# Kernel tuning notes

Measured on AMD Instinct MI355X. Metric: run time of the kernel, lower is better.

## Reference

```python
import jax, jax.numpy as jnp
import numpy as np
from jax import lax

N_LINKS = 10000
N_PATHS = 100000
PATH_LEN = 8   # max_seq_len (all paths padded to this)
H = 32         # link/path state dim and GRU hidden size
RD = 8         # readout dim
T = 8          # message-passing rounds


def setup_inputs() -> dict:
    key = jax.random.key(0)
    ks = jax.random.split(key, 20)
    E = N_PATHS * PATH_LEN
    links = jax.random.randint(ks[0], (E,), 0, N_LINKS)
    paths = jnp.repeat(jnp.arange(N_PATHS), PATH_LEN)
    seqs = jnp.tile(jnp.arange(PATH_LEN), N_PATHS)
    link_capacity = jax.random.uniform(ks[1], (N_LINKS,), dtype=jnp.float32)
    bandwith = jax.random.uniform(ks[2], (N_PATHS,), dtype=jnp.float32)
    s = 1.0 / np.sqrt(H)
    u = lambda k, shp: jax.random.uniform(k, shp, minval=-s, maxval=s, dtype=jnp.float32)
    return {
        'links': links, 'paths': paths, 'seqs': seqs,
        'link_capacity': link_capacity, 'bandwith': bandwith,
        # path GRU (p_U) params, torch layout: [3H, in] with gate order r,z,n
        'p_Wih': u(ks[3], (3 * H, H)), 'p_Whh': u(ks[4], (3 * H, H)),
        'p_bih': u(ks[5], (3 * H,)), 'p_bhh': u(ks[6], (3 * H,)),
        # link GRU (l_U) params
        'l_Wih': u(ks[7], (3 * H, H)), 'l_Whh': u(ks[8], (3 * H, H)),
        'l_bih': u(ks[9], (3 * H,)), 'l_bhh': u(ks[10], (3 * H,)),
        # readout MLP
        'W1': u(ks[11], (RD, H)), 'b1': u(ks[12], (RD,)),
        'W2': u(ks[13], (RD, RD)), 'b2': u(ks[14], (RD,)),
        'W3': u(ks[15], (1, RD)), 'b3': u(ks[16], (1,)),
    }


def gru_cell(x, h, Wih, Whh, bih, bhh):
    # torch GRU cell: gates in order (reset, update, new)
    gi = x @ Wih.T + bih   # [N, 3H]
    gh = h @ Whh.T + bhh   # [N, 3H]
    i_r, i_z, i_n = jnp.split(gi, 3, axis=-1)
    h_r, h_z, h_n = jnp.split(gh, 3, axis=-1)
    r = jax.nn.sigmoid(i_r + h_r)
    z = jax.nn.sigmoid(i_z + h_z)
    n = jnp.tanh(i_n + r * h_n)
    return (1.0 - z) * n + z * h


def reference(links, paths, seqs, link_capacity, bandwith,
              p_Wih, p_Whh, p_bih, p_bhh,
              l_Wih, l_Whh, l_bih, l_bhh,
              W1, b1, W2, b2, W3, b3):
    dt = link_capacity.dtype
    # initial states: feature 0 is capacity / bandwidth, rest zeros
    link_state = jnp.concatenate(
        [link_capacity[:, None], jnp.zeros((N_LINKS, H - 1), dt)], axis=1)
    path_state = jnp.concatenate(
        [bandwith[:, None], jnp.zeros((N_PATHS, H - 1), dt)], axis=1)

    def path_step(h, x_t):
        h2 = gru_cell(x_t, h, p_Wih, p_Whh, p_bih, p_bhh)
        return h2, h2

    for _ in range(T):
        # gather link states onto path hops: [E, H]
        gathered = link_state[links]
        # scatter into dense padded path-RNN input [n_paths, L, H]
        rnn_in = jnp.zeros((N_PATHS, PATH_LEN, H), dt).at[paths, seqs].set(gathered)
        # path GRU over the padded sequence, initial hidden = path_state
        path_state, hs = lax.scan(path_step, path_state,
                                  jnp.swapaxes(rnn_in, 0, 1))  # hs: [L, n_paths, H]
        # per-hop messages back to links, then scatter-add per link
        link_msgs = hs[seqs, paths]                            # [E, H]
        agg = jax.ops.segment_sum(link_msgs, links, num_segments=N_LINKS)
        # link GRU single step: input = aggregated message, hidden = link_state
        link_state = gru_cell(agg, link_state, l_Wih, l_Whh, l_bih, l_bhh)

    # readout MLP on final path state
    x = jax.nn.relu(path_state @ W1.T + b1)
    x = jax.nn.relu(x @ W2.T + b2)
    return x @ W3.T + b3  # [n_paths, 1]
```

## Files before the change

### kernel.cpp

```cpp
#include <hip/hip_runtime.h>
#include <hip/hip_bf16.h>

#define NL 10000
#define NP 100000
#define PLEN 8
#define H 32
#define NROUNDS 8
#define E_TOT (NP * PLEN)

typedef float f2 __attribute__((ext_vector_type(2)));
typedef float f4 __attribute__((ext_vector_type(4)));
typedef short bh8 __attribute__((ext_vector_type(8)));

#define LINK_OFF   0
#define PATH_OFF   320000
#define AGG_OFF    3520000
#define WTS_OFF    3840000
#define PW_OFF     3853400
#define FLAG_OFF   3869000
#define INT_OFF    3870000
#define HS_OFF     4700032
#define WS_NEED_FLOATS (HS_OFF + (size_t)E_TOT * H)

#define LOG2E 1.44269504f

__device__ __forceinline__ float bf2f(unsigned short u) {
  union { unsigned int i; float f; } v; v.i = ((unsigned int)u) << 16; return v.f;
}
__device__ __forceinline__ float fast_exp2(float x) {
#if __has_builtin(__builtin_amdgcn_exp2f)
  return __builtin_amdgcn_exp2f(x);
#else
  return __expf(x * 0.69314718f);
#endif
}
__device__ __forceinline__ float fast_rcp(float x) {
#if __has_builtin(__builtin_amdgcn_rcpf)
  return __builtin_amdgcn_rcpf(x);
#else
  return 1.f / x;
#endif
}
__device__ __forceinline__ float fast_sigm(float x) {
  return fast_rcp(1.f + fast_exp2(-LOG2E * x));
}
__device__ __forceinline__ float fast_tanh2(float x) {
  return 1.f - 2.f * fast_rcp(1.f + fast_exp2((2.f * LOG2E) * x));
}
__device__ __forceinline__ float loadf(const void* p, long i, bool bf) {
  return bf ? bf2f(((const unsigned short*)p)[i]) : ((const float*)p)[i];
}

__device__ __forceinline__ void split8(f4 a, f4 b, bh8& hi, bh8& lo) {
  #pragma unroll
  for (int i = 0; i < 4; ++i) {
    unsigned ua = __float_as_uint(a[i]);
    float hfa = __uint_as_float(ua & 0xffff0000u);
    hi[i] = (short)(ua >> 16);
    lo[i] = (short)(__float_as_uint(a[i] - hfa) >> 16);
    unsigned ub = __float_as_uint(b[i]);
    float hfb = __uint_as_float(ub & 0xffff0000u);
    hi[4 + i] = (short)(ub >> 16);
    lo[4 + i] = (short)(__float_as_uint(b[i] - hfb) >> 16);
  }
}

__global__ void probe_dtype(const unsigned int* __restrict__ cap_words,
                            int* __restrict__ flag) {
  int lane = threadIdx.x;
  int c = 0;
  #pragma unroll
  for (int i = 0; i < 4; ++i) {
    unsigned int b = (cap_words[lane * 4 + i] >> 8) & 0xFF;
    if (b >= 0x30 && b < 0x40) ++c;
  }
  #pragma unroll
  for (int d = 32; d > 0; d >>= 1) c += __shfl_down(c, d);
  if (lane == 0) *flag = (c > 128) ? 1 : 0;
}

__device__ __forceinline__ void gru_cell_f2(const float* __restrict__ W,
                                            const f2 x[16], f2 h[16]) {
  const f2* Wih = (const f2*)W;
  const f2* Whh = (const f2*)(W + 3072);
  const float* bih = W + 6144;
  const float* bhh = W + 6240;
  f2 hn[16];
  #pragma unroll
  for (int jj = 0; jj < 16; ++jj) {
    #pragma unroll
    for (int s = 0; s < 2; ++s) {
      const int j = 2 * jj + s;
      f2 ar = {0.f, 0.f}, az = {0.f, 0.f}, an = {0.f, 0.f}, ah = {0.f, 0.f};
      #pragma unroll
      for (int k = 0; k < 16; ++k) {
        ar = __builtin_elementwise_fma(Wih[j * 16 + k], x[k], ar);
        ar = __builtin_elementwise_fma(Whh[j * 16 + k], h[k], ar);
        az = __builtin_elementwise_fma(Wih[(H + j) * 16 + k], x[k], az);
        az = __builtin_elementwise_fma(Whh[(H + j) * 16 + k], h[k], az);
        an = __builtin_elementwise_fma(Wih[(2 * H + j) * 16 + k], x[k], an);
        ah = __builtin_elementwise_fma(Whh[(2 * H + j) * 16 + k], h[k], ah);
      }
      float r = fast_sigm(ar.x + ar.y + bih[j] + bhh[j]);
      float z = fast_sigm(az.x + az.y + bih[H + j] + bhh[H + j]);
      float n = fast_tanh2(an.x + an.y + bih[2 * H + j] +
                           r * (ah.x + ah.y + bhh[2 * H + j]));
      float hold = (s == 0) ? h[jj].x : h[jj].y;
      float hv = n + z * (hold - n);
      if (s == 0) hn[jj].x = hv; else hn[jj].y = hv;
    }
  }
  #pragma unroll
  for (int k = 0; k < 16; ++k) h[k] = hn[k];
}

struct BfSeg { const void* src; int dstoff; int len; };
struct BfSegs { BfSeg s[14]; };
struct WPack { unsigned short* p[8]; };

__global__ void convert_weights(BfSegs segs, WPack wp, const int* __restrict__ flag,
                                float* __restrict__ dst) {
  const bool bf = (*flag != 0);
  const int si = blockIdx.x;
  const void* p = segs.s[si].src;
  const int off = segs.s[si].dstoff, len = segs.s[si].len;
  int hix = -1;
  if (si == 0) hix = 0; else if (si == 1) hix = 2;
  else if (si == 4) hix = 4; else if (si == 5) hix = 6;
  for (int i = threadIdx.x; i < len; i += blockDim.x) {
    float f = loadf(p, i, bf);
    dst[off + i] = f;
    if (hix >= 0) {
      unsigned u = __float_as_uint(f);
      float fh = __uint_as_float(u & 0xffff0000u);
      wp.p[hix][i] = (unsigned short)(u >> 16);
      wp.p[hix + 1][i] = (unsigned short)(__float_as_uint(f - fh) >> 16);
    }
  }
}

__global__ void init_states(const void* __restrict__ cap,
                            const void* __restrict__ bw,
                            const int* __restrict__ flag,
                            float* __restrict__ link_state,
                            unsigned short* __restrict__ lhi,
                            unsigned short* __restrict__ llo,
                            float* __restrict__ path_state) {
  const bool bf = (*flag != 0);
  int i = blockIdx.x * blockDim.x + threadIdx.x;
  if (i < NP * H) path_state[i] = ((i & (H - 1)) == 0) ? loadf(bw, i >> 5, bf) : 0.f;
  if (i < NL * H) {
    float v = ((i & (H - 1)) == 0) ? loadf(cap, i >> 5, bf) : 0.f;
    link_state[i] = v;
    unsigned u = __float_as_uint(v);
    float fh = __uint_as_float(u & 0xffff0000u);
    lhi[i] = (unsigned short)(u >> 16);
    llo[i] = (unsigned short)(__float_as_uint(v - fh) >> 16);
  }
}

__global__ void csr_count(const int* __restrict__ links, int* __restrict__ counts) {
  int e = blockIdx.x * blockDim.x + threadIdx.x;
  if (e < E_TOT) atomicAdd(&counts[links[e]], 1);
}

__global__ __launch_bounds__(256) void csr_scan(const int* __restrict__ counts,
                                                int* __restrict__ offsets,
                                                int* __restrict__ cursor) {
  __shared__ int part[256];
  const int t = threadIdx.x;
  const int base = t * 40;
  int s = 0;
  for (int i = 0; i < 40; ++i) {
    int idx = base + i;
    if (idx < NL) s += counts[idx];
  }
  part[t] = s;
  __syncthreads();
  for (int d = 1; d < 256; d <<= 1) {
    int v = (t >= d) ? part[t - d] : 0;
    __syncthreads();
    part[t] += v;
    __syncthreads();
  }
  int run = (t > 0) ? part[t - 1] : 0;
  for (int i = 0; i < 40; ++i) {
    int idx = base + i;
    if (idx < NL) {
      offsets[idx] = run;
      cursor[idx] = run;
      run += counts[idx];
    }
  }
  if (t == 255) offsets[NL] = run;
}

__global__ void csr_fill(const int* __restrict__ links, int* __restrict__ cursor,
                         int* __restrict__ edges) {
  int e = blockIdx.x * blockDim.x + threadIdx.x;
  if (e < E_TOT) {
    int l = links[e];
    int pos = atomicAdd(&cursor[l], 1);
    edges[pos] = e;
  }
}

__global__ __launch_bounds__(256) void path_round_mfma(
    const int* __restrict__ links,
    const unsigned short* __restrict__ lhi, const unsigned short* __restrict__ llo,
    float* __restrict__ path_state, float* __restrict__ hs,
    const float* __restrict__ W,
    const unsigned short* __restrict__ wih_hi, const unsigned short* __restrict__ wih_lo,
    const unsigned short* __restrict__ whh_hi, const unsigned short* __restrict__ whh_lo,
    int store_msgs) {
  __shared__ float lds_all[4 * 16 * 36];
  const int wv = threadIdx.x >> 6;
  const int tile = blockIdx.x * 4 + wv;
  if (tile >= NP / 16) return;
  const int p0 = tile * 16;
  const int lane = threadIdx.x & 63;
  const int c = lane & 15, q = lane >> 4, m = c;
  float* lds = lds_all + wv * (16 * 36);

  bh8 wihH[6], wihL[6], whhH[6], whhL[6];
  #pragma unroll
  for (int tn = 0; tn < 6; ++tn) {
    size_t o = (size_t)(tn * 16 + c) * H + q * 8;
    wihH[tn] = *(const bh8*)(wih_hi + o);
    wihL[tn] = *(const bh8*)(wih_lo + o);
    whhH[tn] = *(const bh8*)(whh_hi + o);
    whhL[tn] = *(const bh8*)(whh_lo + o);
  }
  const float* bih = W + 6144;
  const float* bhh = W + 6240;
  f4 bR[2], bZ[2], bI[2], bHn[2];
  #pragma unroll
  for (int u2 = 0; u2 < 2; ++u2) {
    int u = u2 * 16 + c;
    float vr = bih[u] + bhh[u];
    float vz = bih[32 + u] + bhh[32 + u];
    float vi = bih[64 + u];
    float vh = bhh[64 + u];
    bR[u2] = (f4){vr, vr, vr, vr};
    bZ[u2] = (f4){vz, vz, vz, vz};
    bI[u2] = (f4){vi, vi, vi, vi};
    bHn[u2] = (f4){vh, vh, vh, vh};
  }
  float hC[2][4];
  #pragma unroll
  for (int u2 = 0; u2 < 2; ++u2)
    #pragma unroll
    for (int rg = 0; rg < 4; ++rg)
      hC[u2][rg] = path_state[(size_t)(p0 + q * 4 + rg) * H + u2 * 16 + c];
  f4 hfa = *(const f4*)(path_state + (size_t)(p0 + m) * H + q * 8);
  f4 hfb = *(const f4*)(path_state + (size_t)(p0 + m) * H + q * 8 + 4);
  bh8 hhi, hlo;
  split8(hfa, hfb, hhi, hlo);
  int lk[PLEN];
  {
    const int4* lp = (const int4*)(links + (size_t)(p0 + m) * PLEN);
    int4 a = lp[0], b = lp[1];
    lk[0] = a.x; lk[1] = a.y; lk[2] = a.z; lk[3] = a.w;
    lk[4] = b.x; lk[5] = b.y; lk[6] = b.z; lk[7] = b.w;
  }
  bh8 xhi = *(const bh8*)(lhi + (size_t)lk[0] * H + q * 8);
  bh8 xlo = *(const bh8*)(llo + (size_t)lk[0] * H + q * 8);

  #pragma unroll 1
  for (int t = 0; t < PLEN; ++t) {
    bh8 xnhi, xnlo;
    if (t + 1 < PLEN) {
      xnhi = *(const bh8*)(lhi + (size_t)lk[t + 1] * H + q * 8);
      xnlo = *(const bh8*)(llo + (size_t)lk[t + 1] * H + q * 8);
    }
    f4 aR[2], aZ[2], aI[2], aHn[2];
    #pragma unroll
    for (int u2 = 0; u2 < 2; ++u2) {
      f4 a = bR[u2];
      a = __builtin_amdgcn_mfma_f32_16x16x32_bf16(xhi, wihH[u2], a, 0, 0, 0);
      a = __builtin_amdgcn_mfma_f32_16x16x32_bf16(hhi, whhH[u2], a, 0, 0, 0);
      a = __builtin_amdgcn_mfma_f32_16x16x32_bf16(xlo, wihH[u2], a, 0, 0, 0);
      a = __builtin_amdgcn_mfma_f32_16x16x32_bf16(hlo, whhH[u2], a, 0, 0, 0);
      a = __builtin_amdgcn_mfma_f32_16x16x32_bf16(xhi, wihL[u2], a, 0, 0, 0);
      a = __builtin_amdgcn_mfma_f32_16x16x32_bf16(hhi, whhL[u2], a, 0, 0, 0);
      aR[u2] = a;
      f4 b = bZ[u2];
      b = __builtin_amdgcn_mfma_f32_16x16x32_bf16(xhi, wihH[2 + u2], b, 0, 0, 0);
      b = __builtin_amdgcn_mfma_f32_16x16x32_bf16(hhi, whhH[2 + u2], b, 0, 0, 0);
      b = __builtin_amdgcn_mfma_f32_16x16x32_bf16(xlo, wihH[2 + u2], b, 0, 0, 0);
      b = __builtin_amdgcn_mfma_f32_16x16x32_bf16(hlo, whhH[2 + u2], b, 0, 0, 0);
      b = __builtin_amdgcn_mfma_f32_16x16x32_bf16(xhi, wihL[2 + u2], b, 0, 0, 0);
      b = __builtin_amdgcn_mfma_f32_16x16x32_bf16(hhi, whhL[2 + u2], b, 0, 0, 0);
      aZ[u2] = b;
      f4 ci = bI[u2];
      ci = __builtin_amdgcn_mfma_f32_16x16x32_bf16(xhi, wihH[4 + u2], ci, 0, 0, 0);
      ci = __builtin_amdgcn_mfma_f32_16x16x32_bf16(xlo, wihH[4 + u2], ci, 0, 0, 0);
      ci = __builtin_amdgcn_mfma_f32_16x16x32_bf16(xhi, wihL[4 + u2], ci, 0, 0, 0);
      aI[u2] = ci;
      f4 ch = bHn[u2];
      ch = __builtin_amdgcn_mfma_f32_16x16x32_bf16(hhi, whhH[4 + u2], ch, 0, 0, 0);
      ch = __builtin_amdgcn_mfma_f32_16x16x32_bf16(hlo, whhH[4 + u2], ch, 0, 0, 0);
      ch = __builtin_amdgcn_mfma_f32_16x16x32_bf16(hhi, whhL[4 + u2], ch, 0, 0, 0);
      aHn[u2] = ch;
    }
    #pragma unroll
    for (int u2 = 0; u2 < 2; ++u2)
      #pragma unroll
      for (int rg = 0; rg < 4; ++rg) {
        float rr = fast_sigm(aR[u2][rg]);
        float zz = fast_sigm(aZ[u2][rg]);
        float nn = fast_tanh2(fmaf(rr, aHn[u2][rg], aI[u2][rg]));
        float hv = fmaf(zz, hC[u2][rg] - nn, nn);
        hC[u2][rg] = hv;
        lds[(q * 4 + rg) * 36 + u2 * 16 + c] = hv;
      }
    __builtin_amdgcn_wave_barrier();
    __builtin_amdgcn_s_waitcnt(0xC07F);
    f4 ha = *(const f4*)(lds + m * 36 + q * 8);
    f4 hb = *(const f4*)(lds + m * 36 + q * 8 + 4);
    __builtin_amdgcn_wave_barrier();
    if (store_msgs) {
      float* hp = hs + ((size_t)(p0 + m) * PLEN + t) * H + q * 8;
      *(f4*)hp = ha;
      *(f4*)(hp + 4) = hb;
    }
    if (t + 1 < PLEN) {
      split8(ha, hb, hhi, hlo);
      xhi = xnhi; xlo = xnlo;
    } else {
      float* pp = path_state + (size_t)(p0 + m) * H + q * 8;
      *(f4*)pp = ha;
      *(f4*)(pp + 4) = hb;
    }
  }
}

__global__ __launch_bounds__(256) void agg_link_round(
    const int* __restrict__ offsets, const int* __restrict__ edges,
    const float* __restrict__ hs, float* __restrict__ link_state,
    unsigned short* __restrict__ lhi, unsigned short* __restrict__ llo,
    const float* __restrict__ W,
    const unsigned short* __restrict__ wih_hi, const unsigned short* __restrict__ wih_lo,
    const unsigned short* __restrict__ whh_hi, const unsigned short* __restrict__ whh_lo) {
  __shared__ float aggL[16 * 36];
  const int l0 = blockIdx.x * 16;
  const int elem = threadIdx.x & 31;
  #pragma unroll
  for (int li2 = 0; li2 < 2; ++li2) {
    const int li = (threadIdx.x >> 5) + li2 * 8;
    const int l = l0 + li;
    const int beg = offsets[l], end = offsets[l + 1];
    float s0 = 0.f, s1 = 0.f, s2 = 0.f, s3 = 0.f;
    int i = beg;
    for (; i + 3 < end; i += 4) {
      int e0 = edges[i], e1 = edges[i + 1], e2 = edges[i + 2], e3 = edges[i + 3];
      s0 += hs[(size_t)e0 * H + elem];
      s1 += hs[(size_t)e1 * H + elem];
      s2 += hs[(size_t)e2 * H + elem];
      s3 += hs[(size_t)e3 * H + elem];
    }
    for (; i < end; ++i) s0 += hs[(size_t)edges[i] * H + elem];
    aggL[li * 36 + elem] = (s0 + s1) + (s2 + s3);
  }
  __syncthreads();
  if (threadIdx.x >= 64) return;
  const int lane = threadIdx.x;
  const int c = lane & 15, q = lane >> 4, m = c;
  bh8 wihH[6], wihL[6], whhH[6], whhL[6];
  #pragma unroll
  for (int tn = 0; tn < 6; ++tn) {
    size_t o = (size_t)(tn * 16 + c) * H + q * 8;
    wihH[tn] = *(const bh8*)(wih_hi + o);
    wihL[tn] = *(const bh8*)(wih_lo + o);
    whhH[tn] = *(const bh8*)(whh_hi + o);
    whhL[tn] = *(const bh8*)(whh_lo + o);
  }
  const float* bih = W + 6144;
  const float* bhh = W + 6240;
  f4 bR[2], bZ[2], bI[2], bHn[2];
  #pragma unroll
  for (int u2 = 0; u2 < 2; ++u2) {
    int u = u2 * 16 + c;
    float vr = bih[u] + bhh[u];
    float vz = bih[32 + u] + bhh[32 + u];
    float vi = bih[64 + u];
    float vh = bhh[64 + u];
    bR[u2] = (f4){vr, vr, vr, vr};
    bZ[u2] = (f4){vz, vz, vz, vz};
    bI[u2] = (f4){vi, vi, vi, vi};
    bHn[u2] = (f4){vh, vh, vh, vh};
  }
  float hC[2][4];
  #pragma unroll
  for (int u2 = 0; u2 < 2; ++u2)
    #pragma unroll
    for (int rg = 0; rg < 4; ++rg)
      hC[u2][rg] = link_state[(size_t)(l0 + q * 4 + rg) * H + u2 * 16 + c];
  f4 xa = *(const f4*)(aggL + m * 36 + q * 8);
  f4 xb = *(const f4*)(aggL + m * 36 + q * 8 + 4);
  f4 hfa = *(const f4*)(link_state + (size_t)(l0 + m) * H + q * 8);
  f4 hfb = *(const f4*)(link_state + (size_t)(l0 + m) * H + q * 8 + 4);
  bh8 xhi, xlo, hhi, hlo;
  split8(xa, xb, xhi, xlo);
  split8(hfa, hfb, hhi, hlo);
  f4 aR[2], aZ[2], aI[2], aHn[2];
  #pragma unroll
  for (int u2 = 0; u2 < 2; ++u2) {
    f4 a = bR[u2];
    a = __builtin_amdgcn_mfma_f32_16x16x32_bf16(xhi, wihH[u2], a, 0, 0, 0);
    a = __builtin_amdgcn_mfma_f32_16x16x32_bf16(hhi, whhH[u2], a, 0, 0, 0);
    a = __builtin_amdgcn_mfma_f32_16x16x32_bf16(xlo, wihH[u2], a, 0, 0, 0);
    a = __builtin_amdgcn_mfma_f32_16x16x32_bf16(hlo, whhH[u2], a, 0, 0, 0);
    a = __builtin_amdgcn_mfma_f32_16x16x32_bf16(xhi, wihL[u2], a, 0, 0, 0);
    a = __builtin_amdgcn_mfma_f32_16x16x32_bf16(hhi, whhL[u2], a, 0, 0, 0);
    aR[u2] = a;
    f4 b = bZ[u2];
    b = __builtin_amdgcn_mfma_f32_16x16x32_bf16(xhi, wihH[2 + u2], b, 0, 0, 0);
    b = __builtin_amdgcn_mfma_f32_16x16x32_bf16(hhi, whhH[2 + u2], b, 0, 0, 0);
    b = __builtin_amdgcn_mfma_f32_16x16x32_bf16(xlo, wihH[2 + u2], b, 0, 0, 0);
    b = __builtin_amdgcn_mfma_f32_16x16x32_bf16(hlo, whhH[2 + u2], b, 0, 0, 0);
    b = __builtin_amdgcn_mfma_f32_16x16x32_bf16(xhi, wihL[2 + u2], b, 0, 0, 0);
    b = __builtin_amdgcn_mfma_f32_16x16x32_bf16(hhi, whhL[2 + u2], b, 0, 0, 0);
    aZ[u2] = b;
    f4 ci = bI[u2];
    ci = __builtin_amdgcn_mfma_f32_16x16x32_bf16(xhi, wihH[4 + u2], ci, 0, 0, 0);
    ci = __builtin_amdgcn_mfma_f32_16x16x32_bf16(xlo, wihH[4 + u2], ci, 0, 0, 0);
    ci = __builtin_amdgcn_mfma_f32_16x16x32_bf16(xhi, wihL[4 + u2], ci, 0, 0, 0);
    aI[u2] = ci;
    f4 ch = bHn[u2];
    ch = __builtin_amdgcn_mfma_f32_16x16x32_bf16(hhi, whhH[4 + u2], ch, 0, 0, 0);
    ch = __builtin_amdgcn_mfma_f32_16x16x32_bf16(hlo, whhH[4 + u2], ch, 0, 0, 0);
    ch = __builtin_amdgcn_mfma_f32_16x16x32_bf16(hhi, whhL[4 + u2], ch, 0, 0, 0);
    aHn[u2] = ch;
  }
  #pragma unroll
  for (int u2 = 0; u2 < 2; ++u2)
    #pragma unroll
    for (int rg = 0; rg < 4; ++rg) {
      float rr = fast_sigm(aR[u2][rg]);
      float zz = fast_sigm(aZ[u2][rg]);
      float nn = fast_tanh2(fmaf(rr, aHn[u2][rg], aI[u2][rg]));
      float hv = fmaf(zz, hC[u2][rg] - nn, nn);
      size_t idx = (size_t)(l0 + q * 4 + rg) * H + u2 * 16 + c;
      link_state[idx] = hv;
      unsigned u = __float_as_uint(hv);
      float fh = __uint_as_float(u & 0xffff0000u);
      lhi[idx] = (unsigned short)(u >> 16);
      llo[idx] = (unsigned short)(__float_as_uint(hv - fh) >> 16);
    }
}

__global__ __launch_bounds__(64) void path_round_atomic(
    const int* __restrict__ links, const float* __restrict__ link_state,
    float* __restrict__ path_state, float* __restrict__ agg,
    const float* __restrict__ W, int do_scatter) {
  int p = blockIdx.x * 64 + threadIdx.x;
  if (p >= NP) return;
  f2 h[16];
  const f2* ps2 = (const f2*)(path_state + (size_t)p * H);
  #pragma unroll
  for (int k = 0; k < 16; ++k) h[k] = ps2[k];
  int lk[PLEN];
  const int4* lp = (const int4*)(links + (size_t)p * PLEN);
  int4 la = lp[0], lb = lp[1];
  lk[0] = la.x; lk[1] = la.y; lk[2] = la.z; lk[3] = la.w;
  lk[4] = lb.x; lk[5] = lb.y; lk[6] = lb.z; lk[7] = lb.w;
  #pragma unroll 1
  for (int t = 0; t < PLEN; ++t) {
    const f2* xs = (const f2*)(link_state + (size_t)lk[t] * H);
    f2 x[16];
    #pragma unroll
    for (int k = 0; k < 16; ++k) x[k] = xs[k];
    gru_cell_f2(W, x, h);
    if (do_scatter) {
      float* dst = agg + (size_t)lk[t] * H;
      #pragma unroll
      for (int k = 0; k < 16; ++k) {
        unsafeAtomicAdd(dst + 2 * k, h[k].x);
        unsafeAtomicAdd(dst + 2 * k + 1, h[k].y);
      }
    }
  }
  f2* po = (f2*)(path_state + (size_t)p * H);
  #pragma unroll
  for (int k = 0; k < 16; ++k) po[k] = h[k];
}

__global__ __launch_bounds__(64) void link_round_scalar(
    const float* __restrict__ agg, float* __restrict__ link_state,
    const float* __restrict__ W) {
  int li = blockIdx.x * 64 + threadIdx.x;
  if (li >= NL) return;
  f2 x[16], h[16];
  const f2* xa = (const f2*)(agg + (size_t)li * H);
  f2* hsrow = (f2*)(link_state + (size_t)li * H);
  #pragma unroll
  for (int k = 0; k < 16; ++k) { x[k] = xa[k]; h[k] = hsrow[k]; }
  gru_cell_f2(W, x, h);
  #pragma unroll
  for (int k = 0; k < 16; ++k) hsrow[k] = h[k];
}

__global__ __launch_bounds__(256) void readout_kernel(
    const float* __restrict__ path_state, const float* __restrict__ W,
    const int* __restrict__ flag, void* __restrict__ out) {
  int p = blockIdx.x * 256 + threadIdx.x;
  if (p >= NP) return;
  const float* W1 = W;
  const float* b1 = W + 256;
  const float* W2 = W + 264;
  const float* b2 = W + 328;
  const float* W3 = W + 336;
  const float* b3 = W + 344;
  float xv[32];
  const float4* xp = (const float4*)(path_state + (size_t)p * H);
  #pragma unroll
  for (int k = 0; k < 8; ++k) {
    float4 v = xp[k];
    xv[4 * k] = v.x; xv[4 * k + 1] = v.y; xv[4 * k + 2] = v.z; xv[4 * k + 3] = v.w;
  }
  float y1[8];
  #pragma unroll
  for (int i = 0; i < 8; ++i) {
    float a = b1[i];
    #pragma unroll
    for (int k = 0; k < 32; ++k) a = fmaf(W1[i * 32 + k], xv[k], a);
    y1[i] = fmaxf(a, 0.f);
  }
  float y2[8];
  #pragma unroll
  for (int i = 0; i < 8; ++i) {
    float a = b2[i];
    #pragma unroll
    for (int k = 0; k < 8; ++k) a = fmaf(W2[i * 8 + k], y1[k], a);
    y2[i] = fmaxf(a, 0.f);
  }
  float o = b3[0];
  #pragma unroll
  for (int k = 0; k < 8; ++k) o = fmaf(W3[k], y2[k], o);
  if (*flag) ((__hip_bfloat16*)out)[p] = __float2bfloat16(o);
  else       ((float*)out)[p] = o;
}

extern "C" void kernel_launch(void* const* d_in, const int* in_sizes, int n_in,
                              void* d_out, int out_size, void* d_ws, size_t ws_size,
                              hipStream_t stream) {
  (void)in_sizes; (void)n_in; (void)out_size;
  const int* links = (const int*)d_in[0];
  const void* cap = d_in[3];
  const void* bw  = d_in[4];

  float* ws = (float*)d_ws;
  float* link_state = ws + LINK_OFF;
  float* path_state = ws + PATH_OFF;
  float* agg        = ws + AGG_OFF;
  unsigned short* lhi = (unsigned short*)(ws + AGG_OFF);
  unsigned short* llo = (unsigned short*)(ws + AGG_OFF + 160000);
  float* wts        = ws + WTS_OFF;
  int*   flag       = (int*)(ws + FLAG_OFF);
  int*   ibase      = (int*)(ws + INT_OFF);
  int*   counts     = ibase;
  int*   offsets    = ibase + 10000;
  int*   cursor     = ibase + 20016;
  int*   edges      = ibase + 30016;
  float* hs         = ws + HS_OFF;

  WPack wp;
  for (int i = 0; i < 8; ++i)
    wp.p[i] = (unsigned short*)(ws + PW_OFF + i * 1600);

  const bool use_gather = ws_size >= WS_NEED_FLOATS * sizeof(float);

  probe_dtype<<<1, 64, 0, stream>>>((const unsigned int*)cap, flag);

  BfSegs segs;
  const int srcidx[14] = {5, 6, 7, 8, 9, 10, 11, 12, 13, 14, 15, 16, 17, 18};
  const int offs[14]   = {0, 3072, 6144, 6240, 6336, 9408, 12480, 12576,
                          12672, 12928, 12936, 13000, 13008, 13016};
  const int lens[14]   = {3072, 3072, 96, 96, 3072, 3072, 96, 96,
                          256, 8, 64, 8, 8, 1};
  for (int i = 0; i < 14; ++i) {
    segs.s[i].src = d_in[srcidx[i]];
    segs.s[i].dstoff = offs[i];
    segs.s[i].len = lens[i];
  }
  convert_weights<<<14, 256, 0, stream>>>(segs, wp, flag, wts);
  init_states<<<(NP * H + 255) / 256, 256, 0, stream>>>(
      cap, bw, flag, link_state, lhi, llo, path_state);

  if (use_gather) {
    hipMemsetAsync(counts, 0, NL * sizeof(int), stream);
    csr_count<<<(E_TOT + 255) / 256, 256, 0, stream>>>(links, counts);
    csr_scan<<<1, 256, 0, stream>>>(counts, offsets, cursor);
    csr_fill<<<(E_TOT + 255) / 256, 256, 0, stream>>>(links, cursor, edges);

    const int path_blocks = (NP / 16 + 3) / 4;
    for (int r = 0; r < NROUNDS; ++r) {
      const int last = (r == NROUNDS - 1);
      path_round_mfma<<<path_blocks, 256, 0, stream>>>(
          links, lhi, llo, path_state, hs, wts,
          wp.p[0], wp.p[1], wp.p[2], wp.p[3], !last);
      if (!last) {
        agg_link_round<<<NL / 16, 256, 0, stream>>>(
            offsets, edges, hs, link_state, lhi, llo,
            wts + 6336, wp.p[4], wp.p[5], wp.p[6], wp.p[7]);
      }
    }
  } else {
    for (int r = 0; r < NROUNDS; ++r) {
      const int last = (r == NROUNDS - 1);
      if (!last) hipMemsetAsync(agg, 0, NL * H * sizeof(float), stream);
      path_round_atomic<<<(NP + 63) / 64, 64, 0, stream>>>(
          links, link_state, path_state, agg, wts, !last);
      if (!last)
        link_round_scalar<<<(NL + 63) / 64, 64, 0, stream>>>(agg, link_state, wts + 6336);
    }
  }
  readout_kernel<<<(NP + 255) / 256, 256, 0, stream>>>(
      path_state, wts + 12672, flag, d_out);
}
```

Baseline: 903.2 us.

## Scatter path messages into link-sorted order so aggregation reads contiguously

The CSR fill now records, for each edge, its position in link-sorted order instead of an edge list. The path GRU kernel writes each hop's hidden state straight to that sorted slot, so the link aggregation kernel reads a contiguous run per link with no indirect edge lookup. This turns random 128-byte gathers in the aggregation into streaming reads, but makes the path kernel's stores scattered instead of sequential. Separately, the GRU biases are now added in the elementwise stage instead of being used as MFMA accumulator seeds, which frees vector registers at the cost of a few extra adds.

After: 809.6 us. -10.4%, faster.

```diff
diff --git a/kernel.cpp b/kernel.cpp
--- a/kernel.cpp
+++ b/kernel.cpp
@@ -196,17 +196,17 @@
 }
 
 __global__ void csr_fill(const int* __restrict__ links, int* __restrict__ cursor,
-                         int* __restrict__ edges) {
+                         int* __restrict__ perm) {
   int e = blockIdx.x * blockDim.x + threadIdx.x;
   if (e < E_TOT) {
     int l = links[e];
     int pos = atomicAdd(&cursor[l], 1);
-    edges[pos] = e;
+    perm[e] = pos;
   }
 }
 
 __global__ __launch_bounds__(256) void path_round_mfma(
-    const int* __restrict__ links,
+    const int* __restrict__ links, const int* __restrict__ perm,
     const unsigned short* __restrict__ lhi, const unsigned short* __restrict__ llo,
     float* __restrict__ path_state, float* __restrict__ hs,
     const float* __restrict__ W,
@@ -233,18 +233,14 @@
   }
   const float* bih = W + 6144;
   const float* bhh = W + 6240;
-  f4 bR[2], bZ[2], bI[2], bHn[2];
+  float b_r[2], b_z[2], b_in[2], b_hn[2];
   #pragma unroll
   for (int u2 = 0; u2 < 2; ++u2) {
     int u = u2 * 16 + c;
-    float vr = bih[u] + bhh[u];
-    float vz = bih[32 + u] + bhh[32 + u];
-    float vi = bih[64 + u];
-    float vh = bhh[64 + u];
-    bR[u2] = (f4){vr, vr, vr, vr};
-    bZ[u2] = (f4){vz, vz, vz, vz};
-    bI[u2] = (f4){vi, vi, vi, vi};
-    bHn[u2] = (f4){vh, vh, vh, vh};
+    b_r[u2] = bih[u] + bhh[u];
+    b_z[u2] = bih[32 + u] + bhh[32 + u];
+    b_in[u2] = bih[64 + u];
+    b_hn[u2] = bhh[64 + u];
   }
   float hC[2][4];
   #pragma unroll
@@ -256,15 +252,20 @@
   f4 hfb = *(const f4*)(path_state + (size_t)(p0 + m) * H + q * 8 + 4);
   bh8 hhi, hlo;
   split8(hfa, hfb, hhi, hlo);
-  int lk[PLEN];
+  int lk[PLEN], pm[PLEN];
   {
     const int4* lp = (const int4*)(links + (size_t)(p0 + m) * PLEN);
     int4 a = lp[0], b = lp[1];
     lk[0] = a.x; lk[1] = a.y; lk[2] = a.z; lk[3] = a.w;
     lk[4] = b.x; lk[5] = b.y; lk[6] = b.z; lk[7] = b.w;
+    const int4* qp = (const int4*)(perm + (size_t)(p0 + m) * PLEN);
+    int4 e = qp[0], f = qp[1];
+    pm[0] = e.x; pm[1] = e.y; pm[2] = e.z; pm[3] = e.w;
+    pm[4] = f.x; pm[5] = f.y; pm[6] = f.z; pm[7] = f.w;
   }
   bh8 xhi = *(const bh8*)(lhi + (size_t)lk[0] * H + q * 8);
   bh8 xlo = *(const bh8*)(llo + (size_t)lk[0] * H + q * 8);
+  const f4 z4 = {0.f, 0.f, 0.f, 0.f};
 
   #pragma unroll 1
   for (int t = 0; t < PLEN; ++t) {
@@ -276,7 +277,7 @@
     f4 aR[2], aZ[2], aI[2], aHn[2];
     #pragma unroll
     for (int u2 = 0; u2 < 2; ++u2) {
-      f4 a = bR[u2];
+      f4 a = z4;
       a = __builtin_amdgcn_mfma_f32_16x16x32_bf16(xhi, wihH[u2], a, 0, 0, 0);
       a = __builtin_amdgcn_mfma_f32_16x16x32_bf16(hhi, whhH[u2], a, 0, 0, 0);
       a = __builtin_amdgcn_mfma_f32_16x16x32_bf16(xlo, wihH[u2], a, 0, 0, 0);
@@ -284,7 +285,7 @@
       a = __builtin_amdgcn_mfma_f32_16x16x32_bf16(xhi, wihL[u2], a, 0, 0, 0);
       a = __builtin_amdgcn_mfma_f32_16x16x32_bf16(hhi, whhL[u2], a, 0, 0, 0);
       aR[u2] = a;
-      f4 b = bZ[u2];
+      f4 b = z4;
       b = __builtin_amdgcn_mfma_f32_16x16x32_bf16(xhi, wihH[2 + u2], b, 0, 0, 0);
       b = __builtin_amdgcn_mfma_f32_16x16x32_bf16(hhi, whhH[2 + u2], b, 0, 0, 0);
       b = __builtin_amdgcn_mfma_f32_16x16x32_bf16(xlo, wihH[2 + u2], b, 0, 0, 0);
@@ -292,12 +293,12 @@
       b = __builtin_amdgcn_mfma_f32_16x16x32_bf16(xhi, wihL[2 + u2], b, 0, 0, 0);
       b = __builtin_amdgcn_mfma_f32_16x16x32_bf16(hhi, whhL[2 + u2], b, 0, 0, 0);
       aZ[u2] = b;
-      f4 ci = bI[u2];
+      f4 ci = z4;
       ci = __builtin_amdgcn_mfma_f32_16x16x32_bf16(xhi, wihH[4 + u2], ci, 0, 0, 0);
       ci = __builtin_amdgcn_mfma_f32_16x16x32_bf16(xlo, wihH[4 + u2], ci, 0, 0, 0);
       ci = __builtin_amdgcn_mfma_f32_16x16x32_bf16(xhi, wihL[4 + u2], ci, 0, 0, 0);
       aI[u2] = ci;
-      f4 ch = bHn[u2];
+      f4 ch = z4;
       ch = __builtin_amdgcn_mfma_f32_16x16x32_bf16(hhi, whhH[4 + u2], ch, 0, 0, 0);
       ch = __builtin_amdgcn_mfma_f32_16x16x32_bf16(hlo, whhH[4 + u2], ch, 0, 0, 0);
       ch = __builtin_amdgcn_mfma_f32_16x16x32_bf16(hhi, whhL[4 + u2], ch, 0, 0, 0);
@@ -307,9 +308,9 @@
     for (int u2 = 0; u2 < 2; ++u2)
       #pragma unroll
       for (int rg = 0; rg < 4; ++rg) {
-        float rr = fast_sigm(aR[u2][rg]);
-        float zz = fast_sigm(aZ[u2][rg]);
-        float nn = fast_tanh2(fmaf(rr, aHn[u2][rg], aI[u2][rg]));
+        float rr = fast_sigm(aR[u2][rg] + b_r[u2]);
+        float zz = fast_sigm(aZ[u2][rg] + b_z[u2]);
+        float nn = fast_tanh2(fmaf(rr, aHn[u2][rg] + b_hn[u2], aI[u2][rg] + b_in[u2]));
         float hv = fmaf(zz, hC[u2][rg] - nn, nn);
         hC[u2][rg] = hv;
         lds[(q * 4 + rg) * 36 + u2 * 16 + c] = hv;
@@ -320,7 +321,7 @@
     f4 hb = *(const f4*)(lds + m * 36 + q * 8 + 4);
     __builtin_amdgcn_wave_barrier();
     if (store_msgs) {
-      float* hp = hs + ((size_t)(p0 + m) * PLEN + t) * H + q * 8;
+      float* hp = hs + (size_t)pm[t] * H + q * 8;
       *(f4*)hp = ha;
       *(f4*)(hp + 4) = hb;
     }
@@ -336,7 +337,7 @@
 }
 
 __global__ __launch_bounds__(256) void agg_link_round(
-    const int* __restrict__ offsets, const int* __restrict__ edges,
+    const int* __restrict__ offsets,
     const float* __restrict__ hs, float* __restrict__ link_state,
     unsigned short* __restrict__ lhi, unsigned short* __restrict__ llo,
     const float* __restrict__ W,
@@ -350,16 +351,17 @@
     const int li = (threadIdx.x >> 5) + li2 * 8;
     const int l = l0 + li;
     const int beg = offsets[l], end = offsets[l + 1];
+    const float* base = hs + (size_t)beg * H + elem;
+    const int n = end - beg;
     float s0 = 0.f, s1 = 0.f, s2 = 0.f, s3 = 0.f;
-    int i = beg;
-    for (; i + 3 < end; i += 4) {
-      int e0 = edges[i], e1 = edges[i + 1], e2 = edges[i + 2], e3 = edges[i + 3];
-      s0 += hs[(size_t)e0 * H + elem];
-      s1 += hs[(size_t)e1 * H + elem];
-      s2 += hs[(size_t)e2 * H + elem];
-      s3 += hs[(size_t)e3 * H + elem];
-    }
-    for (; i < end; ++i) s0 += hs[(size_t)edges[i] * H + elem];
+    int i = 0;
+    for (; i + 3 < n; i += 4) {
+      s0 += base[(size_t)i * H];
+      s1 += base[(size_t)(i + 1) * H];
+      s2 += base[(size_t)(i + 2) * H];
+      s3 += base[(size_t)(i + 3) * H];
+    }
+    for (; i < n; ++i) s0 += base[(size_t)i * H];
     aggL[li * 36 + elem] = (s0 + s1) + (s2 + s3);
   }
   __syncthreads();
@@ -377,18 +379,14 @@
   }
   const float* bih = W + 6144;
   const float* bhh = W + 6240;
-  f4 bR[2], bZ[2], bI[2], bHn[2];
+  float b_r[2], b_z[2], b_in[2], b_hn[2];
   #pragma unroll
   for (int u2 = 0; u2 < 2; ++u2) {
     int u = u2 * 16 + c;
-    float vr = bih[u] + bhh[u];
-    float vz = bih[32 + u] + bhh[32 + u];
-    float vi = bih[64 + u];
-    float vh = bhh[64 + u];
-    bR[u2] = (f4){vr, vr, vr, vr};
-    bZ[u2] = (f4){vz, vz, vz, vz};
-    bI[u2] = (f4){vi, vi, vi, vi};
-    bHn[u2] = (f4){vh, vh, vh, vh};
+    b_r[u2] = bih[u] + bhh[u];
+    b_z[u2] = bih[32 + u] + bhh[32 + u];
+    b_in[u2] = bih[64 + u];
+    b_hn[u2] = bhh[64 + u];
   }
   float hC[2][4];
   #pragma unroll
@@ -403,10 +401,11 @@
   bh8 xhi, xlo, hhi, hlo;
   split8(xa, xb, xhi, xlo);
   split8(hfa, hfb, hhi, hlo);
+  const f4 z4 = {0.f, 0.f, 0.f, 0.f};
   f4 aR[2], aZ[2], aI[2], aHn[2];
   #pragma unroll
   for (int u2 = 0; u2 < 2; ++u2) {
-    f4 a = bR[u2];
+    f4 a = z4;
     a = __builtin_amdgcn_mfma_f32_16x16x32_bf16(xhi, wihH[u2], a, 0, 0, 0);
     a = __builtin_amdgcn_mfma_f32_16x16x32_bf16(hhi, whhH[u2], a, 0, 0, 0);
     a = __builtin_amdgcn_mfma_f32_16x16x32_bf16(xlo, wihH[u2], a, 0, 0, 0);
@@ -414,7 +413,7 @@
     a = __builtin_amdgcn_mfma_f32_16x16x32_bf16(xhi, wihL[u2], a, 0, 0, 0);
     a = __builtin_amdgcn_mfma_f32_16x16x32_bf16(hhi, whhL[u2], a, 0, 0, 0);
     aR[u2] = a;
-    f4 b = bZ[u2];
+    f4 b = z4;
     b = __builtin_amdgcn_mfma_f32_16x16x32_bf16(xhi, wihH[2 + u2], b, 0, 0, 0);
     b = __builtin_amdgcn_mfma_f32_16x16x32_bf16(hhi, whhH[2 + u2], b, 0, 0, 0);
     b = __builtin_amdgcn_mfma_f32_16x16x32_bf16(xlo, wihH[2 + u2], b, 0, 0, 0);
@@ -422,12 +421,12 @@
     b = __builtin_amdgcn_mfma_f32_16x16x32_bf16(xhi, wihL[2 + u2], b, 0, 0, 0);
     b = __builtin_amdgcn_mfma_f32_16x16x32_bf16(hhi, whhL[2 + u2], b, 0, 0, 0);
     aZ[u2] = b;
-    f4 ci = bI[u2];
+    f4 ci = z4;
     ci = __builtin_amdgcn_mfma_f32_16x16x32_bf16(xhi, wihH[4 + u2], ci, 0, 0, 0);
     ci = __builtin_amdgcn_mfma_f32_16x16x32_bf16(xlo, wihH[4 + u2], ci, 0, 0, 0);
     ci = __builtin_amdgcn_mfma_f32_16x16x32_bf16(xhi, wihL[4 + u2], ci, 0, 0, 0);
     aI[u2] = ci;
-    f4 ch = bHn[u2];
+    f4 ch = z4;
     ch = __builtin_amdgcn_mfma_f32_16x16x32_bf16(hhi, whhH[4 + u2], ch, 0, 0, 0);
     ch = __builtin_amdgcn_mfma_f32_16x16x32_bf16(hlo, whhH[4 + u2], ch, 0, 0, 0);
     ch = __builtin_amdgcn_mfma_f32_16x16x32_bf16(hhi, whhL[4 + u2], ch, 0, 0, 0);
@@ -437,9 +436,9 @@
   for (int u2 = 0; u2 < 2; ++u2)
     #pragma unroll
     for (int rg = 0; rg < 4; ++rg) {
-      float rr = fast_sigm(aR[u2][rg]);
-      float zz = fast_sigm(aZ[u2][rg]);
-      float nn = fast_tanh2(fmaf(rr, aHn[u2][rg], aI[u2][rg]));
+      float rr = fast_sigm(aR[u2][rg] + b_r[u2]);
+      float zz = fast_sigm(aZ[u2][rg] + b_z[u2]);
+      float nn = fast_tanh2(fmaf(rr, aHn[u2][rg] + b_hn[u2], aI[u2][rg] + b_in[u2]));
       float hv = fmaf(zz, hC[u2][rg] - nn, nn);
       size_t idx = (size_t)(l0 + q * 4 + rg) * H + u2 * 16 + c;
       link_state[idx] = hv;
@@ -562,7 +561,7 @@
   int*   counts     = ibase;
   int*   offsets    = ibase + 10000;
   int*   cursor     = ibase + 20016;
-  int*   edges      = ibase + 30016;
+  int*   perm       = ibase + 30016;
   float* hs         = ws + HS_OFF;
 
   WPack wp;
@@ -592,17 +591,17 @@
     hipMemsetAsync(counts, 0, NL * sizeof(int), stream);
     csr_count<<<(E_TOT + 255) / 256, 256, 0, stream>>>(links, counts);
     csr_scan<<<1, 256, 0, stream>>>(counts, offsets, cursor);
-    csr_fill<<<(E_TOT + 255) / 256, 256, 0, stream>>>(links, cursor, edges);
+    csr_fill<<<(E_TOT + 255) / 256, 256, 0, stream>>>(links, cursor, perm);
 
     const int path_blocks = (NP / 16 + 3) / 4;
     for (int r = 0; r < NROUNDS; ++r) {
       const int last = (r == NROUNDS - 1);
       path_round_mfma<<<path_blocks, 256, 0, stream>>>(
-          links, lhi, llo, path_state, hs, wts,
+          links, perm, lhi, llo, path_state, hs, wts,
           wp.p[0], wp.p[1], wp.p[2], wp.p[3], !last);
       if (!last) {
         agg_link_round<<<NL / 16, 256, 0, stream>>>(
-            offsets, edges, hs, link_state, lhi, llo,
+            offsets, hs, link_state, lhi, llo,
             wts + 6336, wp.p[4], wp.p[5], wp.p[6], wp.p[7]);
       }
     }
```
